# Kernel optimization log

Hardware: AMD Instinct MI355X
Metric: run time of the kernel (lower is better)

Reference implementation:

```python
import jax, jax.numpy as jnp
import numpy as np

IN_F = 8192
OUT_F = 8192
MAX_STATES = 100
THRESHOLD = MAX_STATES // 2  # 50


def setup_inputs() -> dict:
    key = jax.random.key(0)
    k1, k2 = jax.random.split(key, 2)
    spike_input = (jax.random.uniform(k1, (IN_F,)) < 0.2).astype(jnp.float32)
    # synapse states as in __init__: randn*5 + threshold, clamped to [1, max_states]
    synapse_states = jnp.clip(
        jax.random.normal(k2, (OUT_F, IN_F)) * 5.0 + THRESHOLD, 1.0, float(MAX_STATES)
    ).astype(jnp.float32)
    membrane_potential = jnp.zeros((OUT_F,), jnp.float32)
    adaptive_threshold = jnp.full((OUT_F,), 3.0, jnp.float32)
    eligibility_trace = jnp.zeros((OUT_F, IN_F), jnp.float32)
    refractory_period = jnp.zeros((OUT_F,), jnp.float32)
    return {
        "spike_input": spike_input,
        "synapse_states": synapse_states,
        "membrane_potential": membrane_potential,
        "adaptive_threshold": adaptive_threshold,
        "eligibility_trace": eligibility_trace,
        "refractory_period": refractory_period,
    }


def reference(spike_input, synapse_states, membrane_potential, adaptive_threshold,
              eligibility_trace, refractory_period):
    # Ternary (effectively binary 0/1) weights from synapse states
    w = (synapse_states > float(THRESHOLD)).astype(jnp.float32)  # [out, in]
    x = spike_input.reshape(-1)                                   # [in]
    current = w @ x                                               # [out]
    # LIF membrane update with refractory gating
    v_mem = membrane_potential * 0.5 + current * (1.0 - refractory_period * 0.5)
    spikes = (v_mem >= adaptive_threshold).astype(jnp.float32)    # [out]
    # Eligibility trace: decay + outer-product accumulation + clamp
    new_trace = jnp.clip(eligibility_trace * 0.8 + jnp.outer(spikes, x), 0.0, 5.0)
    # Refractory update
    new_refractory = jnp.clip(refractory_period + spikes - 0.1, 0.0, 1.0)
    # Membrane reset where spiked
    new_membrane = v_mem * (1.0 - spikes)
    return spikes, new_membrane, new_trace, new_refractory
```

## Files before the change

### kernel.cpp

```cpp
#include <hip/hip_runtime.h>


#define IN_F 8192
#define OUT_F 8192
#define BLOCK 256
#define WAVE_ITERS (IN_F / 4 / 64)

typedef float vfloat4 __attribute__((ext_vector_type(4)));

__global__ __launch_bounds__(BLOCK) void snn_wave_fused_kernel(
    const vfloat4* __restrict__ x4,
    const float* __restrict__ syn,
    const float* __restrict__ mem,
    const float* __restrict__ thr,
    const float* __restrict__ trace,
    const float* __restrict__ refr,
    float* __restrict__ out_spikes,
    float* __restrict__ out_mem,
    float* __restrict__ out_trace,
    float* __restrict__ out_refr)
{
    const int wave = threadIdx.x >> 6;
    const int lane = threadIdx.x & 63;
    const int row  = (blockIdx.x << 2) + wave;

    const vfloat4* __restrict__ syn4 =
        (const vfloat4*)(syn + (size_t)row * IN_F);
    const vfloat4* __restrict__ tr4 =
        (const vfloat4*)(trace + (size_t)row * IN_F);
    vfloat4* __restrict__ otr4 = (vfloat4*)(out_trace + (size_t)row * IN_F);

    float acc = 0.0f;
    #pragma unroll 8
    for (int it = 0; it < WAVE_ITERS; ++it) {
        const int idx = (it << 6) + lane;
        const vfloat4 s  = syn4[idx];
        const vfloat4 xv = x4[idx];
        acc += (s.x > 50.0f) ? xv.x : 0.0f;
        acc += (s.y > 50.0f) ? xv.y : 0.0f;
        acc += (s.z > 50.0f) ? xv.z : 0.0f;
        acc += (s.w > 50.0f) ? xv.w : 0.0f;
    }
    #pragma unroll
    for (int off = 32; off > 0; off >>= 1) {
        acc += __shfl_down(acc, off, 64);
    }
    const float current = __shfl(acc, 0, 64);

    const float r = refr[row];
    const float v = mem[row] * 0.5f + current * (1.0f - r * 0.5f);
    const float spike = (v >= thr[row]) ? 1.0f : 0.0f;
    if (lane == 0) {
        out_spikes[row] = spike;
        out_mem[row]    = v * (1.0f - spike);
        out_refr[row]   = fminf(fmaxf(r + spike - 0.1f, 0.0f), 1.0f);
    }

    #pragma unroll 8
    for (int it = 0; it < WAVE_ITERS; ++it) {
        const int idx = (it << 6) + lane;
        const vfloat4 t  = tr4[idx];
        const vfloat4 xv = x4[idx];
        vfloat4 o;
        o.x = fminf(fmaxf(t.x * 0.8f + spike * xv.x, 0.0f), 5.0f);
        o.y = fminf(fmaxf(t.y * 0.8f + spike * xv.y, 0.0f), 5.0f);
        o.z = fminf(fmaxf(t.z * 0.8f + spike * xv.z, 0.0f), 5.0f);
        o.w = fminf(fmaxf(t.w * 0.8f + spike * xv.w, 0.0f), 5.0f);
        __builtin_nontemporal_store(o, &otr4[idx]);
    }
}

extern "C" void kernel_launch(void* const* d_in, const int* in_sizes, int n_in,
                              void* d_out, int out_size, void* d_ws, size_t ws_size,
                              hipStream_t stream) {
    const float* x_in  = (const float*)d_in[0];
    const float* syn   = (const float*)d_in[1];
    const float* mem   = (const float*)d_in[2];
    const float* thr   = (const float*)d_in[3];
    const float* trace = (const float*)d_in[4];
    const float* refr  = (const float*)d_in[5];

    float* out = (float*)d_out;
    float* out_spikes = out;
    float* out_mem    = out + OUT_F;
    float* out_trace  = out + 2 * OUT_F;
    float* out_refr   = out + 2 * OUT_F + (size_t)OUT_F * IN_F;

    snn_wave_fused_kernel<<<OUT_F / 4, BLOCK, 0, stream>>>(
        (const vfloat4*)x_in, syn, mem, thr, trace, refr,
        out_spikes, out_mem, out_trace, out_refr);
}
```

Before: 599.5 us.

## Bit-pack spike input into LDS and batch synapse and trace loads

A small pre-kernel ballots the spike vector into a 256-word bitmask in workspace. The main kernel copies that mask into shared memory and reads spike bits from it instead of re-reading the float x vector in both passes. Loads of synapse and trace rows are now issued in batches of eight before use, so more memory requests are in flight per wave, and the per-row scalars are loaded early. The cost is one extra kernel launch, plus the assumption that spike_input values are exactly 0 or 1.

```diff
diff --git a/kernel.cpp b/kernel.cpp
--- a/kernel.cpp
+++ b/kernel.cpp
@@ -4,12 +4,26 @@
 #define IN_F 8192
 #define OUT_F 8192
 #define BLOCK 256
-#define WAVE_ITERS (IN_F / 4 / 64)
+#define BATCH 8
+#define NBATCH (IN_F / 4 / 64 / BATCH)
 
 typedef float vfloat4 __attribute__((ext_vector_type(4)));
 
-__global__ __launch_bounds__(BLOCK) void snn_wave_fused_kernel(
-    const vfloat4* __restrict__ x4,
+__global__ __launch_bounds__(BLOCK) void snn_pack_x(
+    const float* __restrict__ x, unsigned long long* __restrict__ mask64)
+{
+    const int wave = threadIdx.x >> 6;
+    const int lane = threadIdx.x & 63;
+    #pragma unroll
+    for (int s = 0; s < 32; ++s) {
+        const float v = x[(wave << 11) + (s << 6) + lane];
+        const unsigned long long b = __ballot(v != 0.0f);
+        if (lane == 0) mask64[(wave << 5) + s] = b;
+    }
+}
+
+__global__ __launch_bounds__(BLOCK) void snn_main_kernel(
+    const unsigned int* __restrict__ xbits,
     const float* __restrict__ syn,
     const float* __restrict__ mem,
     const float* __restrict__ thr,
@@ -20,9 +34,17 @@
     float* __restrict__ out_trace,
     float* __restrict__ out_refr)
 {
+    __shared__ unsigned int sbits[IN_F / 32];
     const int wave = threadIdx.x >> 6;
     const int lane = threadIdx.x & 63;
     const int row  = (blockIdx.x << 2) + wave;
+
+    const float r  = refr[row];
+    const float m0 = mem[row];
+    const float th = thr[row];
+
+    sbits[threadIdx.x] = xbits[threadIdx.x];
+    __syncthreads();
 
     const vfloat4* __restrict__ syn4 =
         (const vfloat4*)(syn + (size_t)row * IN_F);
@@ -31,15 +53,22 @@
     vfloat4* __restrict__ otr4 = (vfloat4*)(out_trace + (size_t)row * IN_F);
 
     float acc = 0.0f;
-    #pragma unroll 8
-    for (int it = 0; it < WAVE_ITERS; ++it) {
-        const int idx = (it << 6) + lane;
-        const vfloat4 s  = syn4[idx];
-        const vfloat4 xv = x4[idx];
-        acc += (s.x > 50.0f) ? xv.x : 0.0f;
-        acc += (s.y > 50.0f) ? xv.y : 0.0f;
-        acc += (s.z > 50.0f) ? xv.z : 0.0f;
-        acc += (s.w > 50.0f) ? xv.w : 0.0f;
+    #pragma unroll
+    for (int ib = 0; ib < NBATCH; ++ib) {
+        vfloat4 s[BATCH];
+        #pragma unroll
+        for (int b = 0; b < BATCH; ++b) {
+            s[b] = syn4[(((ib << 3) + b) << 6) + lane];
+        }
+        #pragma unroll
+        for (int b = 0; b < BATCH; ++b) {
+            const int idx = (((ib << 3) + b) << 6) + lane;
+            const unsigned int bits = sbits[idx >> 3] >> ((idx & 7) << 2);
+            acc += ((s[b].x > 50.0f) && (bits & 1u)) ? 1.0f : 0.0f;
+            acc += ((s[b].y > 50.0f) && (bits & 2u)) ? 1.0f : 0.0f;
+            acc += ((s[b].z > 50.0f) && (bits & 4u)) ? 1.0f : 0.0f;
+            acc += ((s[b].w > 50.0f) && (bits & 8u)) ? 1.0f : 0.0f;
+        }
     }
     #pragma unroll
     for (int off = 32; off > 0; off >>= 1) {
@@ -47,26 +76,32 @@
     }
     const float current = __shfl(acc, 0, 64);
 
-    const float r = refr[row];
-    const float v = mem[row] * 0.5f + current * (1.0f - r * 0.5f);
-    const float spike = (v >= thr[row]) ? 1.0f : 0.0f;
+    const float v = m0 * 0.5f + current * (1.0f - r * 0.5f);
+    const float spike = (v >= th) ? 1.0f : 0.0f;
     if (lane == 0) {
         out_spikes[row] = spike;
         out_mem[row]    = v * (1.0f - spike);
         out_refr[row]   = fminf(fmaxf(r + spike - 0.1f, 0.0f), 1.0f);
     }
 
-    #pragma unroll 8
-    for (int it = 0; it < WAVE_ITERS; ++it) {
-        const int idx = (it << 6) + lane;
-        const vfloat4 t  = tr4[idx];
-        const vfloat4 xv = x4[idx];
-        vfloat4 o;
-        o.x = fminf(fmaxf(t.x * 0.8f + spike * xv.x, 0.0f), 5.0f);
-        o.y = fminf(fmaxf(t.y * 0.8f + spike * xv.y, 0.0f), 5.0f);
-        o.z = fminf(fmaxf(t.z * 0.8f + spike * xv.z, 0.0f), 5.0f);
-        o.w = fminf(fmaxf(t.w * 0.8f + spike * xv.w, 0.0f), 5.0f);
-        __builtin_nontemporal_store(o, &otr4[idx]);
+    #pragma unroll
+    for (int ib = 0; ib < NBATCH; ++ib) {
+        vfloat4 t[BATCH];
+        #pragma unroll
+        for (int b = 0; b < BATCH; ++b) {
+            t[b] = tr4[(((ib << 3) + b) << 6) + lane];
+        }
+        #pragma unroll
+        for (int b = 0; b < BATCH; ++b) {
+            const int idx = (((ib << 3) + b) << 6) + lane;
+            const unsigned int bits = sbits[idx >> 3] >> ((idx & 7) << 2);
+            vfloat4 o;
+            o.x = fminf(fmaxf(t[b].x * 0.8f + ((bits & 1u) ? spike : 0.0f), 0.0f), 5.0f);
+            o.y = fminf(fmaxf(t[b].y * 0.8f + ((bits & 2u) ? spike : 0.0f), 0.0f), 5.0f);
+            o.z = fminf(fmaxf(t[b].z * 0.8f + ((bits & 4u) ? spike : 0.0f), 0.0f), 5.0f);
+            o.w = fminf(fmaxf(t[b].w * 0.8f + ((bits & 8u) ? spike : 0.0f), 0.0f), 5.0f);
+            __builtin_nontemporal_store(o, &otr4[idx]);
+        }
     }
 }
 
@@ -86,7 +121,10 @@
     float* out_trace  = out + 2 * OUT_F;
     float* out_refr   = out + 2 * OUT_F + (size_t)OUT_F * IN_F;
 
-    snn_wave_fused_kernel<<<OUT_F / 4, BLOCK, 0, stream>>>(
-        (const vfloat4*)x_in, syn, mem, thr, trace, refr,
+    snn_pack_x<<<1, BLOCK, 0, stream>>>(
+        x_in, (unsigned long long*)d_ws);
+
+    snn_main_kernel<<<OUT_F / 4, BLOCK, 0, stream>>>(
+        (const unsigned int*)d_ws, syn, mem, thr, trace, refr,
         out_spikes, out_mem, out_trace, out_refr);
 }
```

Result: slower. 614.8 us (+2.6%).

## Split fused kernel into flat grid-stride dot, LIF, and trace kernels

Applied to the files above, without the earlier changes.

Replaces the single row-per-wave fused kernel with three launches: a flat grid-stride kernel that counts active synapses into per-wave partial sums in the workspace, a small LIF kernel that reduces the 32 partials per row and updates the neuron state, and a flat grid-stride trace update kernel. The aim is to spread the large memory streams evenly over a fixed grid with independent loads and to remove the per-row serial dependency between the dot product and the trace pass. The trace stores become ordinary stores instead of nontemporal ones. The cost is two extra launches, a partial-sum round trip through memory, and a per-iteration wave reduction plus scattered partial writes.

```diff
diff --git a/kernel.cpp b/kernel.cpp
--- a/kernel.cpp
+++ b/kernel.cpp
@@ -4,69 +4,81 @@
 #define IN_F 8192
 #define OUT_F 8192
 #define BLOCK 256
-#define WAVE_ITERS (IN_F / 4 / 64)
+#define GRID 2048
+#define TOTAL4 (OUT_F * IN_F / 4)
+#define STRIDE4 (GRID * BLOCK)
+#define ITERS (TOTAL4 / STRIDE4)
 
 typedef float vfloat4 __attribute__((ext_vector_type(4)));
 
-__global__ __launch_bounds__(BLOCK) void snn_wave_fused_kernel(
+__global__ __launch_bounds__(BLOCK) void snn_dot_flat(
+    const vfloat4* __restrict__ syn4,
     const vfloat4* __restrict__ x4,
-    const float* __restrict__ syn,
+    float* __restrict__ partial)
+{
+    const int lane = threadIdx.x & 63;
+    size_t g = (size_t)blockIdx.x * BLOCK + threadIdx.x;
+    #pragma unroll 4
+    for (int k = 0; k < ITERS; ++k, g += STRIDE4) {
+        const vfloat4 s  = syn4[g];
+        const vfloat4 xv = x4[g & 2047];
+        float a = 0.0f;
+        a += ((s.x > 50.0f) && (xv.x != 0.0f)) ? 1.0f : 0.0f;
+        a += ((s.y > 50.0f) && (xv.y != 0.0f)) ? 1.0f : 0.0f;
+        a += ((s.z > 50.0f) && (xv.z != 0.0f)) ? 1.0f : 0.0f;
+        a += ((s.w > 50.0f) && (xv.w != 0.0f)) ? 1.0f : 0.0f;
+        #pragma unroll
+        for (int off = 32; off > 0; off >>= 1) {
+            a += __shfl_down(a, off, 64);
+        }
+        if (lane == 0) partial[g >> 6] = a;
+    }
+}
+
+__global__ __launch_bounds__(BLOCK) void snn_lif(
+    const float* __restrict__ partial,
     const float* __restrict__ mem,
     const float* __restrict__ thr,
-    const float* __restrict__ trace,
     const float* __restrict__ refr,
     float* __restrict__ out_spikes,
     float* __restrict__ out_mem,
-    float* __restrict__ out_trace,
     float* __restrict__ out_refr)
 {
-    const int wave = threadIdx.x >> 6;
-    const int lane = threadIdx.x & 63;
-    const int row  = (blockIdx.x << 2) + wave;
+    const int row = blockIdx.x * BLOCK + threadIdx.x;
+    const vfloat4* __restrict__ p4 =
+        (const vfloat4*)(partial + (size_t)row * 32);
+    float c = 0.0f;
+    #pragma unroll
+    for (int j = 0; j < 8; ++j) {
+        const vfloat4 p = p4[j];
+        c += p.x + p.y + p.z + p.w;
+    }
+    const float r = refr[row];
+    const float v = mem[row] * 0.5f + c * (1.0f - r * 0.5f);
+    const float spike = (v >= thr[row]) ? 1.0f : 0.0f;
+    out_spikes[row] = spike;
+    out_mem[row]    = v * (1.0f - spike);
+    out_refr[row]   = fminf(fmaxf(r + spike - 0.1f, 0.0f), 1.0f);
+}
 
-    const vfloat4* __restrict__ syn4 =
-        (const vfloat4*)(syn + (size_t)row * IN_F);
-    const vfloat4* __restrict__ tr4 =
-        (const vfloat4*)(trace + (size_t)row * IN_F);
-    vfloat4* __restrict__ otr4 = (vfloat4*)(out_trace + (size_t)row * IN_F);
-
-    float acc = 0.0f;
-    #pragma unroll 8
-    for (int it = 0; it < WAVE_ITERS; ++it) {
-        const int idx = (it << 6) + lane;
-        const vfloat4 s  = syn4[idx];
-        const vfloat4 xv = x4[idx];
-        acc += (s.x > 50.0f) ? xv.x : 0.0f;
-        acc += (s.y > 50.0f) ? xv.y : 0.0f;
-        acc += (s.z > 50.0f) ? xv.z : 0.0f;
-        acc += (s.w > 50.0f) ? xv.w : 0.0f;
-    }
-    #pragma unroll
-    for (int off = 32; off > 0; off >>= 1) {
-        acc += __shfl_down(acc, off, 64);
-    }
-    const float current = __shfl(acc, 0, 64);
-
-    const float r = refr[row];
-    const float v = mem[row] * 0.5f + current * (1.0f - r * 0.5f);
-    const float spike = (v >= thr[row]) ? 1.0f : 0.0f;
-    if (lane == 0) {
-        out_spikes[row] = spike;
-        out_mem[row]    = v * (1.0f - spike);
-        out_refr[row]   = fminf(fmaxf(r + spike - 0.1f, 0.0f), 1.0f);
-    }
-
-    #pragma unroll 8
-    for (int it = 0; it < WAVE_ITERS; ++it) {
-        const int idx = (it << 6) + lane;
-        const vfloat4 t  = tr4[idx];
-        const vfloat4 xv = x4[idx];
+__global__ __launch_bounds__(BLOCK) void snn_trace_flat(
+    const vfloat4* __restrict__ tr4,
+    const vfloat4* __restrict__ x4,
+    const float* __restrict__ spikes,
+    vfloat4* __restrict__ otr4)
+{
+    size_t g = (size_t)blockIdx.x * BLOCK + threadIdx.x;
+    #pragma unroll 4
+    for (int k = 0; k < ITERS; ++k, g += STRIDE4) {
+        const float sp   = spikes[g >> 11];
+        const vfloat4 t  = tr4[g];
+        const vfloat4 xv = x4[g & 2047];
         vfloat4 o;
-        o.x = fminf(fmaxf(t.x * 0.8f + spike * xv.x, 0.0f), 5.0f);
-        o.y = fminf(fmaxf(t.y * 0.8f + spike * xv.y, 0.0f), 5.0f);
-        o.z = fminf(fmaxf(t.z * 0.8f + spike * xv.z, 0.0f), 5.0f);
-        o.w = fminf(fmaxf(t.w * 0.8f + spike * xv.w, 0.0f), 5.0f);
-        __builtin_nontemporal_store(o, &otr4[idx]);
+        o.x = fminf(fmaxf(t.x * 0.8f + sp * xv.x, 0.0f), 5.0f);
+        o.y = fminf(fmaxf(t.y * 0.8f + sp * xv.y, 0.0f), 5.0f);
+        o.z = fminf(fmaxf(t.z * 0.8f + sp * xv.z, 0.0f), 5.0f);
+        o.w = fminf(fmaxf(t.w * 0.8f + sp * xv.w, 0.0f), 5.0f);
+        otr4[g] = o;
     }
 }
 
@@ -86,7 +98,15 @@
     float* out_trace  = out + 2 * OUT_F;
     float* out_refr   = out + 2 * OUT_F + (size_t)OUT_F * IN_F;
 
-    snn_wave_fused_kernel<<<OUT_F / 4, BLOCK, 0, stream>>>(
-        (const vfloat4*)x_in, syn, mem, thr, trace, refr,
-        out_spikes, out_mem, out_trace, out_refr);
+    float* partial = (float*)d_ws;
+
+    snn_dot_flat<<<GRID, BLOCK, 0, stream>>>(
+        (const vfloat4*)syn, (const vfloat4*)x_in, partial);
+
+    snn_lif<<<OUT_F / BLOCK, BLOCK, 0, stream>>>(
+        partial, mem, thr, refr, out_spikes, out_mem, out_refr);
+
+    snn_trace_flat<<<GRID, BLOCK, 0, stream>>>(
+        (const vfloat4*)trace, (const vfloat4*)x_in, out_spikes,
+        (vfloat4*)out_trace);
 }
```

New measurement: 602.3 us. About the same (+0.5%).
